# Kernel optimization log

Hardware: AMD Instinct MI355X
Metric: run time of the kernel (lower is better)

Reference implementation:

```python
import jax, jax.numpy as jnp
import numpy as np

DIM = 128
HEADS = 4
HEAD_DIM = DIM // HEADS
WIN = 7
DIL = 1
EPS = 1e-5
HIDDEN = 4 * DIM  # mlp_ratio = 4.0
PAD = DIL * (WIN // 2)


def setup_inputs() -> dict:
    key = jax.random.key(0)
    ks = jax.random.split(key, 16)
    s = 0.02
    return {
        "x": jax.random.normal(ks[0], (8, DIM, 256, 256), dtype=jnp.float32),
        "n1_w": jnp.ones((DIM,), jnp.float32),
        "n1_b": jnp.zeros((DIM,), jnp.float32),
        "qkv_w": jax.random.normal(ks[1], (3 * DIM, DIM), jnp.float32) * s,
        "qkv_b": jnp.zeros((3 * DIM,), jnp.float32),
        "proj_w": jax.random.normal(ks[2], (DIM, DIM), jnp.float32) * s,
        "proj_b": jnp.zeros((DIM,), jnp.float32),
        "n2_w": jnp.ones((DIM,), jnp.float32),
        "n2_b": jnp.zeros((DIM,), jnp.float32),
        "mlp_w1": jax.random.normal(ks[3], (HIDDEN, DIM), jnp.float32) * s,
        "mlp_b1": jnp.zeros((HIDDEN,), jnp.float32),
        "mlp_w2": jax.random.normal(ks[4], (DIM, HIDDEN), jnp.float32) * s,
        "mlp_b2": jnp.zeros((DIM,), jnp.float32),
    }


def _channel_ln(x, w, b):
    # LayerNorm over channel axis (axis=1) of NCHW, per spatial location
    mu = jnp.mean(x, axis=1, keepdims=True)
    var = jnp.mean(jnp.square(x - mu), axis=1, keepdims=True)
    xn = (x - mu) * jax.lax.rsqrt(var + EPS)
    return xn * w[None, :, None, None] + b[None, :, None, None]


def _local_attn(x, qkv_w, qkv_b, proj_w, proj_b):
    B, C, H, W = x.shape
    qkv = jnp.einsum("oc,bchw->bohw", qkv_w, x) + qkv_b[None, :, None, None]
    q, k, v = jnp.split(qkv, 3, axis=1)
    q = q.reshape(B, HEADS, HEAD_DIM, H, W) * (HEAD_DIM ** -0.5)
    k = k.reshape(B, HEADS, HEAD_DIM, H, W)
    v = v.reshape(B, HEADS, HEAD_DIM, H, W)
    # boundary_pad='zeros': pad key/value maps with zeros
    pad = [(0, 0), (0, 0), (0, 0), (PAD, PAD), (PAD, PAD)]
    kp = jnp.pad(k, pad)
    vp = jnp.pad(v, pad)
    offsets = [(oi, oj) for oi in range(WIN) for oj in range(WIN)]
    scores = []
    for oi, oj in offsets:  # fixed small window loop (49 iters)
        ks = kp[..., oi * DIL : oi * DIL + H, oj * DIL : oj * DIL + W]
        scores.append(jnp.einsum("bhcij,bhcij->bhij", q, ks))
    scores = jnp.stack(scores, axis=-1)
    attn = jax.nn.softmax(scores, axis=-1)
    out = jnp.zeros_like(v)
    for idx, (oi, oj) in enumerate(offsets):
        vs = vp[..., oi * DIL : oi * DIL + H, oj * DIL : oj * DIL + W]
        out = out + attn[..., idx][:, :, None] * vs
    out = out.reshape(B, C, H, W)
    return jnp.einsum("oc,bchw->bohw", proj_w, out) + proj_b[None, :, None, None]


def _mlp(x, w1, b1, w2, b2):
    h = jnp.einsum("oc,bchw->bohw", w1, x) + b1[None, :, None, None]
    h = jax.nn.gelu(h)
    return jnp.einsum("oc,bchw->bohw", w2, h) + b2[None, :, None, None]


def reference(x, n1_w, n1_b, qkv_w, qkv_b, proj_w, proj_b, n2_w, n2_b, mlp_w1, mlp_b1, mlp_w2, mlp_b2):
    x = x + _local_attn(_channel_ln(x, n1_w, n1_b), qkv_w, qkv_b, proj_w, proj_b)
    x = x + _mlp(_channel_ln(x, n2_w, n2_b), mlp_w1, mlp_b1, mlp_w2, mlp_b2)
    return x
```

## Files before the change

kernel.cpp:

```cpp
#include <hip/hip_runtime.h>
#include <hip/hip_bf16.h>

typedef unsigned short u16;
typedef unsigned int u32;
typedef __attribute__((ext_vector_type(4))) u32 u32x4;
typedef __attribute__((ext_vector_type(2))) u32 u32x2;
typedef __attribute__((ext_vector_type(8))) __bf16 bf16x8;
typedef __attribute__((ext_vector_type(4))) float f32x4;
typedef __attribute__((ext_vector_type(4))) short short4v;

#define HW 65536
#define MFMA32(a, b, c) __builtin_amdgcn_mfma_f32_16x16x32_bf16((a), (b), (c), 0, 0, 0)

__device__ __forceinline__ u16 f2bf(float f){
  union { u32 i; float f; } v; v.f = f;
  u32 r = v.i + 0x7fffu + ((v.i >> 16) & 1u);
  return (u16)(r >> 16);
}
__device__ __forceinline__ u32 pkbf(float a, float b){
  __bf16 lo = (__bf16)a, hi = (__bf16)b;
  u16 ulo = __builtin_bit_cast(u16, lo);
  u16 uhi = __builtin_bit_cast(u16, hi);
  return (u32)ulo | ((u32)uhi << 16);
}
__device__ __forceinline__ float rcpf(float x){
#if __has_builtin(__builtin_amdgcn_rcpf)
  return __builtin_amdgcn_rcpf(x);
#else
  return 1.0f / x;
#endif
}
__device__ __forceinline__ float gelu_tanh(float v){
  float t = v * v;
  float u = fmaf(0.044715f * t, v, v);
  float z = 1.5957691216057308f * u;
  float e = __expf(-z);
  return v * rcpf(1.0f + e);
}

__device__ __forceinline__ f32x4 mfma16bf16(short4v a, short4v b, f32x4 c){
#if __has_builtin(__builtin_amdgcn_mfma_f32_16x16x16bf16_1k)
  return __builtin_amdgcn_mfma_f32_16x16x16bf16_1k(a, b, c, 0, 0, 0);
#else
  f32x4 d;
  asm volatile("v_mfma_f32_16x16x16_bf16 %0, %1, %2, %3"
               : "=v"(d) : "v"(a), "v"(b), "v"(c));
  return d;
#endif
}

__global__ __launch_bounds__(256) void k_pack(
    const float* __restrict__ qkvw, const float* __restrict__ projw,
    const float* __restrict__ w1, const float* __restrict__ w2,
    u16* __restrict__ wf)
{
  int tile = blockIdx.x;
  int t = threadIdx.x;
  int l = t >> 1, half = t & 1;
  if (l >= 64) return;
  int lg = l >> 4;
  if (tile >= 256){
    int ti = tile - 256;
    int hp = ti >> 3, m = ti & 7;
    int row = m * 16 + (l & 15);
    u16 o[4];
    #pragma unroll
    for (int j = 0; j < 4; ++j){
      int s = half * 4 + j;
      int kloc = (s < 4) ? (4 * lg + s) : (16 + 4 * lg + (s - 4));
      o[j] = f2bf(w2[(size_t)row * 512 + hp * 32 + kloc]);
    }
    u32x2 v; v[0] = (u32)o[0] | ((u32)o[1] << 16); v[1] = (u32)o[2] | ((u32)o[3] << 16);
    *(u32x2*)(wf + 131072 + ti * 512 + l * 8 + half * 4) = v;
    return;
  }
  const float* W; int base, ti;
  if (tile < 96)       { W = qkvw; base = 0;     ti = tile; }
  else if (tile < 128) { W = projw; base = 49152; ti = tile - 96; }
  else                 { W = w1;   base = 65536; ti = tile - 128; }
  int mt = ti / 4, kt = ti % 4;
  int r0 = half * 4;
  int m = mt * 16 + (l & 15);
  int kb = kt * 32 + 8 * lg + r0;
  u16 o[4];
  #pragma unroll
  for (int j = 0; j < 4; ++j) o[j] = f2bf(W[(size_t)m * 128 + kb + j]);
  u32x2 v; v[0] = (u32)o[0] | ((u32)o[1] << 16); v[1] = (u32)o[2] | ((u32)o[3] << 16);
  *(u32x2*)(wf + base + ti * 512 + l * 8 + r0) = v;
}

__global__ __launch_bounds__(256, 2) void k_ln_qkv(
    const float* __restrict__ x, const float* __restrict__ n1w,
    const float* __restrict__ n1b, const u16* __restrict__ wfq,
    const float* __restrict__ qkvb, u16* __restrict__ qkvp)
{
  __shared__ __align__(16) char smem[66560];
  float* red  = (float*)(smem + 16384);
  float* mu_s = (float*)(smem + 18432);
  float* rs_s = (float*)(smem + 18688);

  const int t = threadIdx.x;
  const int w = t >> 6, l = t & 63;
  const int P0 = blockIdx.x * 64;
  const int b = P0 >> 16;
  const int pix0 = P0 & 65535;
  const float* xb = x + ((size_t)b * 128) * HW + pix0 + l;

  float xv[32];
  float s = 0.f, s2 = 0.f;
  #pragma unroll
  for (int j = 0; j < 32; ++j){
    float v = xb[(size_t)(w * 32 + j) * HW];
    xv[j] = v; s += v; s2 += v * v;
  }
  red[w * 64 + l] = s;
  red[256 + w * 64 + l] = s2;
  __syncthreads();
  if (t < 64){
    float ss  = red[t] + red[64 + t] + red[128 + t] + red[192 + t];
    float ss2 = red[256 + t] + red[320 + t] + red[384 + t] + red[448 + t];
    float mu = ss * 0.0078125f;
    float var = ss2 * 0.0078125f - mu * mu;
    mu_s[t] = mu; rs_s[t] = rsqrtf(var + 1e-5f);
  }
  __syncthreads();
  {
    float mu = mu_s[l], rs = rs_s[l];
    #pragma unroll
    for (int jj = 0; jj < 4; ++jj){
      int c0 = w * 32 + jj * 8;
      u32x4 pk;
      #pragma unroll
      for (int k2 = 0; k2 < 4; ++k2){
        float v0 = (xv[jj*8 + k2*2    ] - mu) * rs * n1w[c0 + k2*2    ] + n1b[c0 + k2*2    ];
        float v1 = (xv[jj*8 + k2*2 + 1] - mu) * rs * n1w[c0 + k2*2 + 1] + n1b[c0 + k2*2 + 1];
        pk[k2] = pkbf(v0, v1);
      }
      *(u32x4*)(smem + l * 256 + (((w * 4 + jj) ^ (l & 7)) << 4)) = pk;
    }
  }
  __syncthreads();

  const int lg = l >> 4, ln = l & 15;
  const bf16x8* wfrag = (const bf16x8*)wfq;
  f32x4 acc[6][4];
  #pragma unroll
  for (int m = 0; m < 6; ++m)
    #pragma unroll
    for (int n = 0; n < 4; ++n) acc[m][n] = (f32x4)(0.f);
  #pragma unroll
  for (int kt = 0; kt < 4; ++kt){
    bf16x8 a[6], bb[4];
    #pragma unroll
    for (int m = 0; m < 6; ++m) a[m] = wfrag[((w*6 + m)*4 + kt)*64 + l];
    #pragma unroll
    for (int n = 0; n < 4; ++n){
      int p = n * 16 + ln;
      bb[n] = *(const bf16x8*)(smem + p * 256 + ((((kt*4 + lg)) ^ (p & 7)) << 4));
    }
    #pragma unroll
    for (int m = 0; m < 6; ++m)
      #pragma unroll
      for (int n = 0; n < 4; ++n)
        acc[m][n] = MFMA32(a[m], bb[n], acc[m][n]);
  }
  #pragma unroll
  for (int m = 0; m < 6; ++m)
    #pragma unroll
    for (int n = 0; n < 4; ++n){
      int o0 = w * 96 + m * 16 + 4 * lg;
      float qs = (o0 < 128) ? 0.17677669529663687f : 1.0f;
      int p = n * 16 + ln;
      u32x2 v;
      v[0] = pkbf((acc[m][n][0] + qkvb[o0+0]) * qs, (acc[m][n][1] + qkvb[o0+1]) * qs);
      v[1] = pkbf((acc[m][n][2] + qkvb[o0+2]) * qs, (acc[m][n][3] + qkvb[o0+3]) * qs);
      *(u32x2*)(smem + 16384 + p * 784 + o0 * 2) = v;
    }
  __syncthreads();
  for (int i = t; i < 3072; i += 256){
    int p = i / 48, c8 = i - p * 48;
    u32x4 v = *(const u32x4*)(smem + 16384 + p * 784 + c8 * 16);
    int sel = c8 >> 4, hh = (c8 >> 2) & 3, c0 = (c8 & 3) * 8;
    u16* plane = qkvp + (size_t)sel * 67108864ull;
    *(u32x4*)(plane + (((size_t)(b*4 + hh)) * 65536 + pix0 + p) * 32 + c0) = v;
  }
}

__global__ __launch_bounds__(256, 2) void k_attn(
    u16* qbuf, const u16* __restrict__ kbuf, const u16* __restrict__ vbuf)
{
  __shared__ __align__(16) u16 Klds[4 * 512 * 8];
  __shared__ __align__(16) u16 VT[32 * 532 + 16];
  const int t = threadIdx.x;
  const int blk = blockIdx.x;
  const int tx16 = blk & 15, ty16 = (blk >> 4) & 15;
  const int h = (blk >> 8) & 3, b = blk >> 10;
  const int y0 = ty16 * 16, x0 = tx16 * 16;
  const int bh = b * 4 + h;
  const u16* kg = kbuf + (size_t)bh * 65536 * 32;
  const u16* vg = vbuf + (size_t)bh * 65536 * 32;

  for (int i = t; i < 2130; i += 256) ((u32x4*)VT)[i] = (u32x4){0u,0u,0u,0u};
  __syncthreads();

  for (int pix = t; pix < 484; pix += 256){
    int yy = pix / 22, xx = pix - yy * 22;
    int gy = y0 + yy - 3, gx = x0 + xx - 3;
    bool ok = (gy >= 0 && gy < 256 && gx >= 0 && gx < 256);
    u32x4 kv[4], vv[4];
    #pragma unroll
    for (int j = 0; j < 4; ++j){ kv[j] = (u32x4){0u,0u,0u,0u}; vv[j] = (u32x4){0u,0u,0u,0u}; }
    if (ok){
      size_t gb = ((size_t)(gy * 256 + gx)) * 32;
      #pragma unroll
      for (int j = 0; j < 4; ++j){
        kv[j] = *(const u32x4*)(kg + gb + j * 8);
        vv[j] = *(const u32x4*)(vg + gb + j * 8);
      }
    }
    #pragma unroll
    for (int j = 0; j < 4; ++j)
      *(u32x4*)(Klds + (j * 512 + pix) * 8) = kv[j];
    int vb = yy * 24 + xx;
    #pragma unroll
    for (int j = 0; j < 4; ++j)
      #pragma unroll
      for (int ww = 0; ww < 4; ++ww){
        int c = j * 8 + ww * 2;
        VT[(c    ) * 532 + vb] = (u16)(vv[j][ww] & 0xffffu);
        VT[(c + 1) * 532 + vb] = (u16)(vv[j][ww] >> 16);
      }
  }
  __syncthreads();

  const int l = t & 63, w = t >> 6;
  const int ln = l & 15, g = l >> 4;

  bool mk[2][4];
  #pragma unroll
  for (int sl = 0; sl < 2; ++sl)
    #pragma unroll
    for (int r = 0; r < 4; ++r)
      mk[sl][r] = ((unsigned)(sl * 16 + g * 4 + r - ln)) <= 6u;

  for (int rt = 0; rt < 4; ++rt){
    int yl = rt * 4 + w;
    int qpix = (y0 + yl) * 256 + x0 + ln;
    u16* qp = qbuf + ((size_t)bh * 65536 + qpix) * 32;
    bf16x8 qf = *(const bf16x8*)(qp + g * 8);

    f32x4 S[7][2];
    #pragma unroll
    for (int oi = 0; oi < 7; ++oi){
      int rowb = (yl + oi) * 22;
      #pragma unroll
      for (int sl = 0; sl < 2; ++sl){
        bf16x8 kf = *(const bf16x8*)(Klds + (g * 512 + rowb + sl * 16 + ln) * 8);
        f32x4 z = (f32x4)(0.f);
        S[oi][sl] = MFMA32(kf, qf, z);
      }
    }
    float m = -3e38f;
    #pragma unroll
    for (int oi = 0; oi < 7; ++oi)
      #pragma unroll
      for (int sl = 0; sl < 2; ++sl)
        #pragma unroll
        for (int r = 0; r < 4; ++r){
          float v = mk[sl][r] ? S[oi][sl][r] : -3e38f;
          S[oi][sl][r] = v;
          m = fmaxf(m, v);
        }
    m = fmaxf(m, __shfl_xor(m, 16));
    m = fmaxf(m, __shfl_xor(m, 32));
    float sum = 0.f;
    #pragma unroll
    for (int oi = 0; oi < 7; ++oi)
      #pragma unroll
      for (int sl = 0; sl < 2; ++sl)
        #pragma unroll
        for (int r = 0; r < 4; ++r){
          float e = __expf(S[oi][sl][r] - m);
          S[oi][sl][r] = e;
          sum += e;
        }
    sum += __shfl_xor(sum, 16);
    sum += __shfl_xor(sum, 32);
    float inv = 1.f / sum;

    short4v P[7][2];
    #pragma unroll
    for (int oi = 0; oi < 7; ++oi)
      #pragma unroll
      for (int sl = 0; sl < 2; ++sl){
        union { u32x2 u; short4v s; } cv;
        cv.u[0] = pkbf(S[oi][sl][0], S[oi][sl][1]);
        cv.u[1] = pkbf(S[oi][sl][2], S[oi][sl][3]);
        P[oi][sl] = cv.s;
      }

    f32x4 O0 = (f32x4)(0.f), O1 = (f32x4)(0.f);
    #pragma unroll
    for (int oi = 0; oi < 7; ++oi){
      int rowE = (yl + oi) * 24;
      #pragma unroll
      for (int sl = 0; sl < 2; ++sl){
        int xb = rowE + sl * 16 + 4 * g;
        short4v v0 = *(const short4v*)(VT + (ln     ) * 532 + xb);
        short4v v1 = *(const short4v*)(VT + (ln + 16) * 532 + xb);
        O0 = mfma16bf16(v0, P[oi][sl], O0);
        O1 = mfma16bf16(v1, P[oi][sl], O1);
      }
    }
    u32x2 o0, o1;
    o0[0] = pkbf(O0[0]*inv, O0[1]*inv);
    o0[1] = pkbf(O0[2]*inv, O0[3]*inv);
    o1[0] = pkbf(O1[0]*inv, O1[1]*inv);
    o1[1] = pkbf(O1[2]*inv, O1[3]*inv);
    *(u32x2*)(qp + 4 * g)      = o0;
    *(u32x2*)(qp + 16 + 4 * g) = o1;
  }
}

__global__ __launch_bounds__(256, 2) void k_proj_mlp(
    const u16* __restrict__ ao, const u16* __restrict__ wfp,
    const float* __restrict__ projb, const float* __restrict__ x,
    const float* __restrict__ n2w, const float* __restrict__ n2b,
    const u16* __restrict__ wf1, const float* __restrict__ b1,
    const u16* __restrict__ wf2, const float* __restrict__ b2,
    float* __restrict__ yout)
{
  __shared__ __align__(16) char smem[65536];
  const int t = threadIdx.x;
  const int w = t >> 6, l = t & 63, lg = l >> 4, ln = l & 15;
  const int P0 = blockIdx.x * 128;
  const int b = P0 >> 16;
  const int pix0 = P0 & 65535;

  auto stage16k = [&](const u16* gsrc, int ldsoff){
    const char* g = (const char*)gsrc;
    int base = w * 4096;
    #pragma unroll
    for (int i = 0; i < 4; ++i){
      int off = base + i * 1024;
      __builtin_amdgcn_global_load_lds(
        (const __attribute__((address_space(1))) u32*)(g + off + l * 16),
        (__attribute__((address_space(3))) u32*)(smem + ldsoff + off),
        16, 0, 0);
    }
  };

  stage16k(wfp, 32768);
  stage16k(wfp + 8192, 49152);
  #pragma unroll
  for (int half = 0; half < 2; ++half){
    int p4 = half * 64 + (t >> 2), c4 = t & 3;
    #pragma unroll
    for (int hh = 0; hh < 4; ++hh){
      int ch = hh * 4 + c4;
      u32x4 v = *(const u32x4*)(ao + (((size_t)(b*4 + hh)) * 65536 + pix0 + p4) * 32 + c4 * 8);
      *(u32x4*)(smem + p4 * 256 + ((ch ^ (p4 & 7)) << 4)) = v;
    }
  }
  __syncthreads();

  const int pA = w * 32 + ln;
  const int pB = pA + 16;

  bf16x8 bbA[4], bbB[4];
  #pragma unroll
  for (int kt = 0; kt < 4; ++kt){
    bbA[kt] = *(const bf16x8*)(smem + pA * 256 + (((kt*4 + lg) ^ (pA & 7)) << 4));
    bbB[kt] = *(const bf16x8*)(smem + pB * 256 + (((kt*4 + lg) ^ (pB & 7)) << 4));
  }

  f32x4 yvA[8], yvB[8];
  #pragma unroll
  for (int m = 0; m < 8; ++m){ yvA[m] = (f32x4)(0.f); yvB[m] = (f32x4)(0.f); }
  #pragma unroll
  for (int kt = 0; kt < 4; ++kt)
    #pragma unroll
    for (int m = 0; m < 8; ++m){
      bf16x8 a = *(const bf16x8*)(smem + 32768 + ((m*4 + kt) << 10) + l * 16);
      yvA[m] = MFMA32(a, bbA[kt], yvA[m]);
      yvB[m] = MFMA32(a, bbB[kt], yvB[m]);
    }
  __syncthreads();
  stage16k(wf1, 32768);
  stage16k(wf2, 49152);

  float sA = 0.f, s2A = 0.f, sB = 0.f, s2B = 0.f;
  #pragma unroll
  for (int m = 0; m < 8; ++m){
    int c0 = m * 16 + 4 * lg;
    f32x4 pbv = *(const f32x4*)(projb + c0);
    size_t baseA = ((size_t)(b * 128 + c0)) * HW + pix0 + pA;
    #pragma unroll
    for (int r = 0; r < 4; ++r){
      float vA = x[baseA + (size_t)r * HW] + yvA[m][r] + pbv[r];
      float vB = x[baseA + 16 + (size_t)r * HW] + yvB[m][r] + pbv[r];
      yvA[m][r] = vA; yvB[m][r] = vB;
      sA += vA; s2A = fmaf(vA, vA, s2A);
      sB += vB; s2B = fmaf(vB, vB, s2B);
    }
  }
  sA  += __shfl_xor(sA, 16);  sA  += __shfl_xor(sA, 32);
  s2A += __shfl_xor(s2A, 16); s2A += __shfl_xor(s2A, 32);
  sB  += __shfl_xor(sB, 16);  sB  += __shfl_xor(sB, 32);
  s2B += __shfl_xor(s2B, 16); s2B += __shfl_xor(s2B, 32);
  float muA = sA * 0.0078125f;
  float rsA = rsqrtf(s2A * 0.0078125f - muA * muA + 1e-5f);
  float muB = sB * 0.0078125f;
  float rsB = rsqrtf(s2B * 0.0078125f - muB * muB + 1e-5f);

  #pragma unroll
  for (int m = 0; m < 8; ++m){
    int c0 = m * 16 + 4 * lg;
    f32x4 wv = *(const f32x4*)(n2w + c0);
    f32x4 bv = *(const f32x4*)(n2b + c0);
    int g8 = c0 >> 3;
    u32x2 pkA, pkB;
    pkA[0] = pkbf((yvA[m][0]-muA)*rsA*wv[0]+bv[0], (yvA[m][1]-muA)*rsA*wv[1]+bv[1]);
    pkA[1] = pkbf((yvA[m][2]-muA)*rsA*wv[2]+bv[2], (yvA[m][3]-muA)*rsA*wv[3]+bv[3]);
    pkB[0] = pkbf((yvB[m][0]-muB)*rsB*wv[0]+bv[0], (yvB[m][1]-muB)*rsB*wv[1]+bv[1]);
    pkB[1] = pkbf((yvB[m][2]-muB)*rsB*wv[2]+bv[2], (yvB[m][3]-muB)*rsB*wv[3]+bv[3]);
    *(u32x2*)(smem + pA * 256 + ((g8 ^ (pA & 7)) << 4) + ((lg & 1) << 3)) = pkA;
    *(u32x2*)(smem + pB * 256 + ((g8 ^ (pB & 7)) << 4) + ((lg & 1) << 3)) = pkB;
  }
  #pragma unroll
  for (int kt = 0; kt < 4; ++kt){
    bbA[kt] = *(const bf16x8*)(smem + pA * 256 + (((kt*4 + lg) ^ (pA & 7)) << 4));
    bbB[kt] = *(const bf16x8*)(smem + pB * 256 + (((kt*4 + lg) ^ (pB & 7)) << 4));
  }
  __syncthreads();

  f32x4 acA[8], acB[8];
  #pragma unroll
  for (int m = 0; m < 8; ++m){ acA[m] = (f32x4)(0.f); acB[m] = (f32x4)(0.f); }

  for (int c = 0; c < 8; ++c){
    const int curoff = (c & 1) ? 0 : 32768;
    if (c < 7){
      const int nxt = curoff ^ 32768;
      stage16k(wf1 + (c + 1) * 8192, nxt);
      stage16k(wf2 + (c + 1) * 8192, nxt + 16384);
    }
    f32x4 hA[4], hB[4];
    #pragma unroll
    for (int mt = 0; mt < 4; ++mt){ hA[mt] = (f32x4)(0.f); hB[mt] = (f32x4)(0.f); }
    #pragma unroll
    for (int kt = 0; kt < 4; ++kt)
      #pragma unroll
      for (int mt = 0; mt < 4; ++mt){
        bf16x8 a = *(const bf16x8*)(smem + curoff + ((mt*4 + kt) << 10) + l * 16);
        hA[mt] = MFMA32(a, bbA[kt], hA[mt]);
        hB[mt] = MFMA32(a, bbB[kt], hB[mt]);
      }
    int hb0 = c * 64 + 4 * lg;
    f32x4 b1v[4];
    #pragma unroll
    for (int mt = 0; mt < 4; ++mt) b1v[mt] = *(const f32x4*)(b1 + hb0 + mt * 16);
    bf16x8 hfA0, hfA1, hfB0, hfB1;
    {
      union { u32x4 u; bf16x8 h; } uu;
      uu.u[0] = pkbf(gelu_tanh(hA[0][0]+b1v[0][0]), gelu_tanh(hA[0][1]+b1v[0][1]));
      uu.u[1] = pkbf(gelu_tanh(hA[0][2]+b1v[0][2]), gelu_tanh(hA[0][3]+b1v[0][3]));
      uu.u[2] = pkbf(gelu_tanh(hA[1][0]+b1v[1][0]), gelu_tanh(hA[1][1]+b1v[1][1]));
      uu.u[3] = pkbf(gelu_tanh(hA[1][2]+b1v[1][2]), gelu_tanh(hA[1][3]+b1v[1][3]));
      hfA0 = uu.h;
      uu.u[0] = pkbf(gelu_tanh(hA[2][0]+b1v[2][0]), gelu_tanh(hA[2][1]+b1v[2][1]));
      uu.u[1] = pkbf(gelu_tanh(hA[2][2]+b1v[2][2]), gelu_tanh(hA[2][3]+b1v[2][3]));
      uu.u[2] = pkbf(gelu_tanh(hA[3][0]+b1v[3][0]), gelu_tanh(hA[3][1]+b1v[3][1]));
      uu.u[3] = pkbf(gelu_tanh(hA[3][2]+b1v[3][2]), gelu_tanh(hA[3][3]+b1v[3][3]));
      hfA1 = uu.h;
      uu.u[0] = pkbf(gelu_tanh(hB[0][0]+b1v[0][0]), gelu_tanh(hB[0][1]+b1v[0][1]));
      uu.u[1] = pkbf(gelu_tanh(hB[0][2]+b1v[0][2]), gelu_tanh(hB[0][3]+b1v[0][3]));
      uu.u[2] = pkbf(gelu_tanh(hB[1][0]+b1v[1][0]), gelu_tanh(hB[1][1]+b1v[1][1]));
      uu.u[3] = pkbf(gelu_tanh(hB[1][2]+b1v[1][2]), gelu_tanh(hB[1][3]+b1v[1][3]));
      hfB0 = uu.h;
      uu.u[0] = pkbf(gelu_tanh(hB[2][0]+b1v[2][0]), gelu_tanh(hB[2][1]+b1v[2][1]));
      uu.u[1] = pkbf(gelu_tanh(hB[2][2]+b1v[2][2]), gelu_tanh(hB[2][3]+b1v[2][3]));
      uu.u[2] = pkbf(gelu_tanh(hB[3][0]+b1v[3][0]), gelu_tanh(hB[3][1]+b1v[3][1]));
      uu.u[3] = pkbf(gelu_tanh(hB[3][2]+b1v[3][2]), gelu_tanh(hB[3][3]+b1v[3][3]));
      hfB1 = uu.h;
    }
    #pragma unroll
    for (int hpl = 0; hpl < 2; ++hpl)
      #pragma unroll
      for (int m = 0; m < 8; ++m){
        bf16x8 a = *(const bf16x8*)(smem + curoff + 16384 + ((hpl*8 + m) << 10) + l * 16);
        acA[m] = MFMA32(a, hpl ? hfA1 : hfA0, acA[m]);
        acB[m] = MFMA32(a, hpl ? hfB1 : hfB0, acB[m]);
      }
    if (c < 7) __syncthreads();
  }

  #pragma unroll
  for (int m = 0; m < 8; ++m){
    int c0 = m * 16 + 4 * lg;
    f32x4 b2v = *(const f32x4*)(b2 + c0);
    size_t baseA = ((size_t)(b * 128 + c0)) * HW + pix0 + pA;
    #pragma unroll
    for (int r = 0; r < 4; ++r){
      yout[baseA + (size_t)r * HW]      = yvA[m][r] + acA[m][r] + b2v[r];
      yout[baseA + 16 + (size_t)r * HW] = yvB[m][r] + acB[m][r] + b2v[r];
    }
  }
}

extern "C" void kernel_launch(void* const* d_in, const int* in_sizes, int n_in,
                              void* d_out, int out_size, void* d_ws, size_t ws_size,
                              hipStream_t stream)
{
  const float* x    = (const float*)d_in[0];
  const float* n1w  = (const float*)d_in[1];
  const float* n1b  = (const float*)d_in[2];
  const float* qkvw = (const float*)d_in[3];
  const float* qkvb = (const float*)d_in[4];
  const float* pw   = (const float*)d_in[5];
  const float* pb   = (const float*)d_in[6];
  const float* n2w  = (const float*)d_in[7];
  const float* n2b  = (const float*)d_in[8];
  const float* w1   = (const float*)d_in[9];
  const float* b1   = (const float*)d_in[10];
  const float* w2   = (const float*)d_in[11];
  const float* b2   = (const float*)d_in[12];

  u16* qkvp = (u16*)d_ws;
  u16* qbuf = qkvp;
  u16* kbuf = qkvp + 67108864ull;
  u16* vbuf = qkvp + 134217728ull;
  u16* wf   = qkvp + 201326592ull;
  u16* wfq = wf;
  u16* wfp = wf + 49152;
  u16* wf1 = wf + 65536;
  u16* wf2 = wf + 131072;
  float* y = (float*)d_out;

  k_pack<<<384, 256, 0, stream>>>(qkvw, pw, w1, w2, wf);
  k_ln_qkv<<<8192, 256, 0, stream>>>(x, n1w, n1b, wfq, qkvb, qkvp);
  k_attn<<<8192, 256, 0, stream>>>(qbuf, kbuf, vbuf);
  k_proj_mlp<<<4096, 256, 0, stream>>>(qbuf, wfp, pb, x, n2w, n2b, wf1, b1, wf2, b2, y);
}
```

Measured before the change: 685.4 us.

## Halve proj/MLP kernel LDS to raise occupancy and remap attention block order

```diff
diff --git a/kernel.cpp b/kernel.cpp
--- a/kernel.cpp
+++ b/kernel.cpp
@@ -192,7 +192,7 @@
   __shared__ __align__(16) u16 Klds[4 * 512 * 8];
   __shared__ __align__(16) u16 VT[32 * 532 + 16];
   const int t = threadIdx.x;
-  const int blk = blockIdx.x;
+  const int blk = ((blockIdx.x & 7) << 10) | (blockIdx.x >> 3);
   const int tx16 = blk & 15, ty16 = (blk >> 4) & 15;
   const int h = (blk >> 8) & 3, b = blk >> 10;
   const int y0 = ty16 * 16, x0 = tx16 * 16;
@@ -322,7 +322,7 @@
   }
 }
 
-__global__ __launch_bounds__(256, 2) void k_proj_mlp(
+__global__ __launch_bounds__(256, 3) void k_proj_mlp(
     const u16* __restrict__ ao, const u16* __restrict__ wfp,
     const float* __restrict__ projb, const float* __restrict__ x,
     const float* __restrict__ n2w, const float* __restrict__ n2b,
@@ -330,39 +330,30 @@
     const u16* __restrict__ wf2, const float* __restrict__ b2,
     float* __restrict__ yout)
 {
-  __shared__ __align__(16) char smem[65536];
+  __shared__ __align__(16) char smem[32768];
   const int t = threadIdx.x;
   const int w = t >> 6, l = t & 63, lg = l >> 4, ln = l & 15;
   const int P0 = blockIdx.x * 128;
   const int b = P0 >> 16;
   const int pix0 = P0 & 65535;
 
-  auto stage16k = [&](const u16* gsrc, int ldsoff){
+  auto stage8k = [&](const u16* gsrc, int ldsoff){
     const char* g = (const char*)gsrc;
-    int base = w * 4096;
-    #pragma unroll
-    for (int i = 0; i < 4; ++i){
+    int base = w * 2048;
+    #pragma unroll
+    for (int i = 0; i < 2; ++i){
       int off = base + i * 1024;
       __builtin_amdgcn_global_load_lds(
-        (const __attribute__((address_space(1))) u32*)(g + off + l * 16),
-        (__attribute__((address_space(3))) u32*)(smem + ldsoff + off),
+        (const u32 __attribute__((address_space(1)))*)(g + off + l * 16),
+        (u32 __attribute__((address_space(3)))*)(smem + ldsoff + off),
         16, 0, 0);
     }
   };
 
-  stage16k(wfp, 32768);
-  stage16k(wfp + 8192, 49152);
-  #pragma unroll
-  for (int half = 0; half < 2; ++half){
-    int p4 = half * 64 + (t >> 2), c4 = t & 3;
-    #pragma unroll
-    for (int hh = 0; hh < 4; ++hh){
-      int ch = hh * 4 + c4;
-      u32x4 v = *(const u32x4*)(ao + (((size_t)(b*4 + hh)) * 65536 + pix0 + p4) * 32 + c4 * 8);
-      *(u32x4*)(smem + p4 * 256 + ((ch ^ (p4 & 7)) << 4)) = v;
-    }
-  }
-  __syncthreads();
+  stage8k(wfp,          0);
+  stage8k(wfp + 4096,   8192);
+  stage8k(wfp + 8192,  16384);
+  stage8k(wfp + 12288, 24576);
 
   const int pA = w * 32 + ln;
   const int pB = pA + 16;
@@ -370,9 +361,22 @@
   bf16x8 bbA[4], bbB[4];
   #pragma unroll
   for (int kt = 0; kt < 4; ++kt){
-    bbA[kt] = *(const bf16x8*)(smem + pA * 256 + (((kt*4 + lg) ^ (pA & 7)) << 4));
-    bbB[kt] = *(const bf16x8*)(smem + pB * 256 + (((kt*4 + lg) ^ (pB & 7)) << 4));
-  }
+    const u16* hb = ao + ((size_t)(b * 4 + kt)) * 2097152ull;
+    bbA[kt] = *(const bf16x8*)(hb + (size_t)(pix0 + pA) * 32 + lg * 8);
+    bbB[kt] = *(const bf16x8*)(hb + (size_t)(pix0 + pB) * 32 + lg * 8);
+  }
+  float xrA[8][4], xrB[8][4];
+  #pragma unroll
+  for (int m = 0; m < 8; ++m){
+    int c0 = m * 16 + 4 * lg;
+    size_t base = ((size_t)(b * 128 + c0)) * HW + pix0 + pA;
+    #pragma unroll
+    for (int r = 0; r < 4; ++r){
+      xrA[m][r] = x[base + (size_t)r * HW];
+      xrB[m][r] = x[base + 16 + (size_t)r * HW];
+    }
+  }
+  __syncthreads();
 
   f32x4 yvA[8], yvB[8];
   #pragma unroll
@@ -381,24 +385,24 @@
   for (int kt = 0; kt < 4; ++kt)
     #pragma unroll
     for (int m = 0; m < 8; ++m){
-      bf16x8 a = *(const bf16x8*)(smem + 32768 + ((m*4 + kt) << 10) + l * 16);
+      int off = (m < 4) ? ((m*4 + kt) << 10) : (16384 + (((m-4)*4 + kt) << 10));
+      bf16x8 a = *(const bf16x8*)(smem + off + l * 16);
       yvA[m] = MFMA32(a, bbA[kt], yvA[m]);
       yvB[m] = MFMA32(a, bbB[kt], yvB[m]);
     }
   __syncthreads();
-  stage16k(wf1, 32768);
-  stage16k(wf2, 49152);
+  stage8k(wf1, 0);
+  stage8k(wf2, 8192);
 
   float sA = 0.f, s2A = 0.f, sB = 0.f, s2B = 0.f;
   #pragma unroll
   for (int m = 0; m < 8; ++m){
     int c0 = m * 16 + 4 * lg;
     f32x4 pbv = *(const f32x4*)(projb + c0);
-    size_t baseA = ((size_t)(b * 128 + c0)) * HW + pix0 + pA;
     #pragma unroll
     for (int r = 0; r < 4; ++r){
-      float vA = x[baseA + (size_t)r * HW] + yvA[m][r] + pbv[r];
-      float vB = x[baseA + 16 + (size_t)r * HW] + yvB[m][r] + pbv[r];
+      float vA = xrA[m][r] + yvA[m][r] + pbv[r];
+      float vB = xrB[m][r] + yvB[m][r] + pbv[r];
       yvA[m][r] = vA; yvB[m][r] = vB;
       sA += vA; s2A = fmaf(vA, vA, s2A);
       sB += vB; s2B = fmaf(vB, vB, s2B);
@@ -413,97 +417,103 @@
   float muB = sB * 0.0078125f;
   float rsB = rsqrtf(s2B * 0.0078125f - muB * muB + 1e-5f);
 
-  #pragma unroll
-  for (int m = 0; m < 8; ++m){
-    int c0 = m * 16 + 4 * lg;
-    f32x4 wv = *(const f32x4*)(n2w + c0);
-    f32x4 bv = *(const f32x4*)(n2b + c0);
-    int g8 = c0 >> 3;
-    u32x2 pkA, pkB;
-    pkA[0] = pkbf((yvA[m][0]-muA)*rsA*wv[0]+bv[0], (yvA[m][1]-muA)*rsA*wv[1]+bv[1]);
-    pkA[1] = pkbf((yvA[m][2]-muA)*rsA*wv[2]+bv[2], (yvA[m][3]-muA)*rsA*wv[3]+bv[3]);
-    pkB[0] = pkbf((yvB[m][0]-muB)*rsB*wv[0]+bv[0], (yvB[m][1]-muB)*rsB*wv[1]+bv[1]);
-    pkB[1] = pkbf((yvB[m][2]-muB)*rsB*wv[2]+bv[2], (yvB[m][3]-muB)*rsB*wv[3]+bv[3]);
-    *(u32x2*)(smem + pA * 256 + ((g8 ^ (pA & 7)) << 4) + ((lg & 1) << 3)) = pkA;
-    *(u32x2*)(smem + pB * 256 + ((g8 ^ (pB & 7)) << 4) + ((lg & 1) << 3)) = pkB;
-  }
-  #pragma unroll
-  for (int kt = 0; kt < 4; ++kt){
-    bbA[kt] = *(const bf16x8*)(smem + pA * 256 + (((kt*4 + lg) ^ (pA & 7)) << 4));
-    bbB[kt] = *(const bf16x8*)(smem + pB * 256 + (((kt*4 + lg) ^ (pB & 7)) << 4));
-  }
-  __syncthreads();
+  {
+    char* wbase = smem + 16384 + w * 4096;
+    #pragma unroll
+    for (int m = 0; m < 8; ++m){
+      int c0 = m * 16 + 4 * lg;
+      f32x4 wv = *(const f32x4*)(n2w + c0);
+      f32x4 bv = *(const f32x4*)(n2b + c0);
+      int g8 = c0 >> 3;
+      u32x2 pk;
+      pk[0] = pkbf((yvA[m][0]-muA)*rsA*wv[0]+bv[0], (yvA[m][1]-muA)*rsA*wv[1]+bv[1]);
+      pk[1] = pkbf((yvA[m][2]-muA)*rsA*wv[2]+bv[2], (yvA[m][3]-muA)*rsA*wv[3]+bv[3]);
+      *(u32x2*)(wbase + ln * 256 + ((g8 ^ (ln & 7)) << 4) + ((lg & 1) << 3)) = pk;
+    }
+    #pragma unroll
+    for (int kt = 0; kt < 4; ++kt)
+      bbA[kt] = *(const bf16x8*)(wbase + ln * 256 + (((kt*4 + lg) ^ (ln & 7)) << 4));
+    #pragma unroll
+    for (int m = 0; m < 8; ++m){
+      int c0 = m * 16 + 4 * lg;
+      f32x4 wv = *(const f32x4*)(n2w + c0);
+      f32x4 bv = *(const f32x4*)(n2b + c0);
+      int g8 = c0 >> 3;
+      u32x2 pk;
+      pk[0] = pkbf((yvB[m][0]-muB)*rsB*wv[0]+bv[0], (yvB[m][1]-muB)*rsB*wv[1]+bv[1]);
+      pk[1] = pkbf((yvB[m][2]-muB)*rsB*wv[2]+bv[2], (yvB[m][3]-muB)*rsB*wv[3]+bv[3]);
+      *(u32x2*)(wbase + ln * 256 + ((g8 ^ (ln & 7)) << 4) + ((lg & 1) << 3)) = pk;
+    }
+    #pragma unroll
+    for (int kt = 0; kt < 4; ++kt)
+      bbB[kt] = *(const bf16x8*)(wbase + ln * 256 + (((kt*4 + lg) ^ (ln & 7)) << 4));
+  }
 
   f32x4 acA[8], acB[8];
-  #pragma unroll
-  for (int m = 0; m < 8; ++m){ acA[m] = (f32x4)(0.f); acB[m] = (f32x4)(0.f); }
-
-  for (int c = 0; c < 8; ++c){
-    const int curoff = (c & 1) ? 0 : 32768;
-    if (c < 7){
-      const int nxt = curoff ^ 32768;
-      stage16k(wf1 + (c + 1) * 8192, nxt);
-      stage16k(wf2 + (c + 1) * 8192, nxt + 16384);
-    }
-    f32x4 hA[4], hB[4];
-    #pragma unroll
-    for (int mt = 0; mt < 4; ++mt){ hA[mt] = (f32x4)(0.f); hB[mt] = (f32x4)(0.f); }
-    #pragma unroll
-    for (int kt = 0; kt < 4; ++kt)
-      #pragma unroll
-      for (int mt = 0; mt < 4; ++mt){
-        bf16x8 a = *(const bf16x8*)(smem + curoff + ((mt*4 + kt) << 10) + l * 16);
-        hA[mt] = MFMA32(a, bbA[kt], hA[mt]);
-        hB[mt] = MFMA32(a, bbB[kt], hB[mt]);
-      }
-    int hb0 = c * 64 + 4 * lg;
-    f32x4 b1v[4];
-    #pragma unroll
-    for (int mt = 0; mt < 4; ++mt) b1v[mt] = *(const f32x4*)(b1 + hb0 + mt * 16);
-    bf16x8 hfA0, hfA1, hfB0, hfB1;
-    {
-      union { u32x4 u; bf16x8 h; } uu;
-      uu.u[0] = pkbf(gelu_tanh(hA[0][0]+b1v[0][0]), gelu_tanh(hA[0][1]+b1v[0][1]));
-      uu.u[1] = pkbf(gelu_tanh(hA[0][2]+b1v[0][2]), gelu_tanh(hA[0][3]+b1v[0][3]));
-      uu.u[2] = pkbf(gelu_tanh(hA[1][0]+b1v[1][0]), gelu_tanh(hA[1][1]+b1v[1][1]));
-      uu.u[3] = pkbf(gelu_tanh(hA[1][2]+b1v[1][2]), gelu_tanh(hA[1][3]+b1v[1][3]));
-      hfA0 = uu.h;
-      uu.u[0] = pkbf(gelu_tanh(hA[2][0]+b1v[2][0]), gelu_tanh(hA[2][1]+b1v[2][1]));
-      uu.u[1] = pkbf(gelu_tanh(hA[2][2]+b1v[2][2]), gelu_tanh(hA[2][3]+b1v[2][3]));
-      uu.u[2] = pkbf(gelu_tanh(hA[3][0]+b1v[3][0]), gelu_tanh(hA[3][1]+b1v[3][1]));
-      uu.u[3] = pkbf(gelu_tanh(hA[3][2]+b1v[3][2]), gelu_tanh(hA[3][3]+b1v[3][3]));
-      hfA1 = uu.h;
-      uu.u[0] = pkbf(gelu_tanh(hB[0][0]+b1v[0][0]), gelu_tanh(hB[0][1]+b1v[0][1]));
-      uu.u[1] = pkbf(gelu_tanh(hB[0][2]+b1v[0][2]), gelu_tanh(hB[0][3]+b1v[0][3]));
-      uu.u[2] = pkbf(gelu_tanh(hB[1][0]+b1v[1][0]), gelu_tanh(hB[1][1]+b1v[1][1]));
-      uu.u[3] = pkbf(gelu_tanh(hB[1][2]+b1v[1][2]), gelu_tanh(hB[1][3]+b1v[1][3]));
-      hfB0 = uu.h;
-      uu.u[0] = pkbf(gelu_tanh(hB[2][0]+b1v[2][0]), gelu_tanh(hB[2][1]+b1v[2][1]));
-      uu.u[1] = pkbf(gelu_tanh(hB[2][2]+b1v[2][2]), gelu_tanh(hB[2][3]+b1v[2][3]));
-      uu.u[2] = pkbf(gelu_tanh(hB[3][0]+b1v[3][0]), gelu_tanh(hB[3][1]+b1v[3][1]));
-      uu.u[3] = pkbf(gelu_tanh(hB[3][2]+b1v[3][2]), gelu_tanh(hB[3][3]+b1v[3][3]));
-      hfB1 = uu.h;
-    }
-    #pragma unroll
-    for (int hpl = 0; hpl < 2; ++hpl)
-      #pragma unroll
-      for (int m = 0; m < 8; ++m){
-        bf16x8 a = *(const bf16x8*)(smem + curoff + 16384 + ((hpl*8 + m) << 10) + l * 16);
-        acA[m] = MFMA32(a, hpl ? hfA1 : hfA0, acA[m]);
-        acB[m] = MFMA32(a, hpl ? hfB1 : hfB0, acB[m]);
-      }
-    if (c < 7) __syncthreads();
-  }
-
   #pragma unroll
   for (int m = 0; m < 8; ++m){
     int c0 = m * 16 + 4 * lg;
     f32x4 b2v = *(const f32x4*)(b2 + c0);
-    size_t baseA = ((size_t)(b * 128 + c0)) * HW + pix0 + pA;
     #pragma unroll
     for (int r = 0; r < 4; ++r){
-      yout[baseA + (size_t)r * HW]      = yvA[m][r] + acA[m][r] + b2v[r];
-      yout[baseA + 16 + (size_t)r * HW] = yvB[m][r] + acB[m][r] + b2v[r];
+      acA[m][r] = yvA[m][r] + b2v[r];
+      acB[m][r] = yvB[m][r] + b2v[r];
+    }
+  }
+  __syncthreads();
+
+  for (int c = 0; c < 16; ++c){
+    const int cur = (c & 1) ? 16384 : 0;
+    if (c < 15){
+      const int nxt = cur ^ 16384;
+      stage8k(wf1 + (c + 1) * 4096, nxt);
+      stage8k(wf2 + (c + 1) * 4096, nxt + 8192);
+    }
+    f32x4 hA[2], hB[2];
+    hA[0] = (f32x4)(0.f); hA[1] = (f32x4)(0.f);
+    hB[0] = (f32x4)(0.f); hB[1] = (f32x4)(0.f);
+    #pragma unroll
+    for (int kt = 0; kt < 4; ++kt)
+      #pragma unroll
+      for (int mt = 0; mt < 2; ++mt){
+        bf16x8 a = *(const bf16x8*)(smem + cur + ((mt*4 + kt) << 10) + l * 16);
+        hA[mt] = MFMA32(a, bbA[kt], hA[mt]);
+        hB[mt] = MFMA32(a, bbB[kt], hB[mt]);
+      }
+    int hb0 = c * 32 + 4 * lg;
+    f32x4 b1a = *(const f32x4*)(b1 + hb0);
+    f32x4 b1b = *(const f32x4*)(b1 + hb0 + 16);
+    bf16x8 hfA, hfB;
+    {
+      union { u32x4 u; bf16x8 h; } uu;
+      uu.u[0] = pkbf(gelu_tanh(hA[0][0]+b1a[0]), gelu_tanh(hA[0][1]+b1a[1]));
+      uu.u[1] = pkbf(gelu_tanh(hA[0][2]+b1a[2]), gelu_tanh(hA[0][3]+b1a[3]));
+      uu.u[2] = pkbf(gelu_tanh(hA[1][0]+b1b[0]), gelu_tanh(hA[1][1]+b1b[1]));
+      uu.u[3] = pkbf(gelu_tanh(hA[1][2]+b1b[2]), gelu_tanh(hA[1][3]+b1b[3]));
+      hfA = uu.h;
+      uu.u[0] = pkbf(gelu_tanh(hB[0][0]+b1a[0]), gelu_tanh(hB[0][1]+b1a[1]));
+      uu.u[1] = pkbf(gelu_tanh(hB[0][2]+b1a[2]), gelu_tanh(hB[0][3]+b1a[3]));
+      uu.u[2] = pkbf(gelu_tanh(hB[1][0]+b1b[0]), gelu_tanh(hB[1][1]+b1b[1]));
+      uu.u[3] = pkbf(gelu_tanh(hB[1][2]+b1b[2]), gelu_tanh(hB[1][3]+b1b[3]));
+      hfB = uu.h;
+    }
+    #pragma unroll
+    for (int m = 0; m < 8; ++m){
+      bf16x8 a = *(const bf16x8*)(smem + cur + 8192 + (m << 10) + l * 16);
+      acA[m] = MFMA32(a, hfA, acA[m]);
+      acB[m] = MFMA32(a, hfB, acB[m]);
+    }
+    if (c < 15) __syncthreads();
+  }
+
+  #pragma unroll
+  for (int m = 0; m < 8; ++m){
+    int c0 = m * 16 + 4 * lg;
+    size_t base = ((size_t)(b * 128 + c0)) * HW + pix0 + pA;
+    #pragma unroll
+    for (int r = 0; r < 4; ++r){
+      yout[base + (size_t)r * HW]      = acA[m][r];
+      yout[base + 16 + (size_t)r * HW] = acB[m][r];
     }
   }
 }
```

Result: no change. 693.5 us (+1.2%).
